# Optimization experiments

Hardware: AMD Instinct MI355X
Metric: run time of the kernel (lower is better)

Reference implementation:

```python
import jax, jax.numpy as jnp
import numpy as np

N_EXPERTS = 8
TOPK = 2
D_MODEL = 2048
D_FF = 2048
N_TOKENS = 8192
FP8_MAX = 448.0  # float8_e4m3fn max


def _fp8_quant_scalar(w):
    # per-tensor (scalar) fp8 quantization, as fp8_quantize(weight, scalar=True)
    amax = jnp.max(jnp.abs(w))
    scale = jnp.maximum(amax, 1e-12) / FP8_MAX
    q = (w / scale).astype(jnp.float8_e4m3fn).astype(jnp.float32)
    return q, scale


def _fp8_qdq_st(x):
    # dynamic_quant(x, single_scale=True) followed by inline dequant,
    # with straight-through estimator so fwd/bwd modules share math.
    amax = jnp.max(jnp.abs(x))
    scale = jnp.maximum(amax, 1e-12) / FP8_MAX
    qdq = (x / scale).astype(jnp.float8_e4m3fn).astype(jnp.float32) * scale
    return x + jax.lax.stop_gradient(qdq - x)


def setup_inputs() -> dict:
    key = jax.random.key(0)
    k1, k2, k3, k4 = jax.random.split(key, 4)
    x = jax.random.normal(k1, (N_TOKENS, D_MODEL), dtype=jnp.float32)
    gating_output = jax.random.normal(k2, (N_TOKENS, N_EXPERTS), dtype=jnp.float32)
    # per-expert fused gate+up weight [E, 2*d_ff, d_model], down weight [E, d_model, d_ff]
    w13 = jax.random.normal(k3, (N_EXPERTS, 2 * D_FF, D_MODEL), dtype=jnp.float32) * 0.02
    w2 = jax.random.normal(k4, (N_EXPERTS, D_MODEL, D_FF), dtype=jnp.float32) * 0.02
    w13_q, w13_scale = jax.vmap(_fp8_quant_scalar)(w13)
    w2_q, w2_scale = jax.vmap(_fp8_quant_scalar)(w2)
    return {
        "x": x,
        "gating_output": gating_output,
        "w13_q": w13_q,
        "w13_scale": w13_scale,
        "w2_q": w2_q,
        "w2_scale": w2_scale,
    }


def reference(x, gating_output, w13_q, w13_scale, w2_q, w2_scale):
    # --- select_experts: softmax scoring, top-k, renormalize ---
    probs = jax.nn.softmax(gating_output, axis=-1)              # [T, E]
    topk_w, topk_ids = jax.lax.top_k(probs, TOPK)               # [T, K]
    topk_w = topk_w / jnp.sum(topk_w, axis=-1, keepdims=True)   # renormalize=True

    # --- dynamic fp8 quantize + dequant of hidden states (single scale) ---
    x_dq = _fp8_qdq_st(x)                                       # [T, D]

    out = jnp.zeros((x.shape[0], D_MODEL), dtype=jnp.float32)
    for e in range(N_EXPERTS):
        # combine weight per token for this expert
        combine = jnp.sum(jnp.where(topk_ids == e, topk_w, 0.0), axis=-1)  # [T]
        w13 = w13_q[e] * w13_scale[e]                            # dequant [2F, D]
        w2 = w2_q[e] * w2_scale[e]                               # dequant [D, F]
        gu = x_dq @ w13.T                                        # [T, 2F]
        gate, up = gu[:, :D_FF], gu[:, D_FF:]
        h = jax.nn.silu(gate) * up                               # [T, F]
        out = out + combine[:, None] * (h @ w2.T)                # [T, D]
    return out
```

## Files before the change

### kernel.cpp

```cpp
#include <hip/hip_runtime.h>
#include <stdint.h>

#define T_TOK 8192
#define DM    2048
#define DFF   2048

typedef __attribute__((ext_vector_type(8))) short bf16x8;
typedef __attribute__((ext_vector_type(4))) float f32x4;

#define OFF_AMAX  0
#define OFF_CNT   64
#define OFF_PBASE 128
#define OFF_TMETA 192
#define OFF_TSE   256
#define OFF_TM0   960
#define OFF_BTOK  4096
#define OFF_BW    (OFF_BTOK + 16*T_TOK*4)
#define OFF_XQ    (2*1024*1024)
#define OFF_W13B  (OFF_XQ + T_TOK*DM*2)
#define OFF_W2B   (OFF_W13B + 8*2*DFF*DM*2)
#define OFF_H     (OFF_W2B + 8*DM*DFF*2)

#define GP(p) ((const __attribute__((address_space(1))) void*)(uintptr_t)(p))
#define LP(p) ((__attribute__((address_space(3))) void*)(uint32_t)(uintptr_t)(p))

__device__ __forceinline__ short bf16_rne(float f) {
    uint32_t b = __float_as_uint(f);
    b += 0x7FFFu + ((b >> 16) & 1u);
    return (short)(b >> 16);
}

__device__ __forceinline__ float fp8_round(float y) {
    float a = fabsf(y);
    a = fminf(a, 448.f);
    uint32_t b = __float_as_uint(a);
    if (b >= 0x3C800000u) {
        uint32_t lsb = (b >> 20) & 1u;
        b += 0x7FFFFu + lsb;
        b &= 0xFFF00000u;
        a = __uint_as_float(b);
    } else {
        a = rintf(a * 512.f) * (1.f / 512.f);
    }
    return (y < 0.f) ? -a : a;
}

__global__ void k_amax(const float4* __restrict__ x, unsigned* __restrict__ amax) {
    __shared__ float red[256];
    float m = 0.f;
    const int n4 = T_TOK * DM / 4;
    for (int i = blockIdx.x * blockDim.x + threadIdx.x; i < n4; i += gridDim.x * blockDim.x) {
        float4 v = x[i];
        m = fmaxf(m, fmaxf(fmaxf(fabsf(v.x), fabsf(v.y)), fmaxf(fabsf(v.z), fabsf(v.w))));
    }
    red[threadIdx.x] = m;
    __syncthreads();
    for (int s = 128; s > 0; s >>= 1) {
        if (threadIdx.x < s) red[threadIdx.x] = fmaxf(red[threadIdx.x], red[threadIdx.x + s]);
        __syncthreads();
    }
    if (threadIdx.x == 0) atomicMax(amax, __float_as_uint(red[0]));
}

__global__ void k_router(const float* __restrict__ gating, int* __restrict__ cnt,
                         int* __restrict__ btok, float* __restrict__ bw) {
    int t = blockIdx.x * blockDim.x + threadIdx.x;
    if (t >= T_TOK) return;
    float l[8], p[8];
    float lmax = -1e30f;
#pragma unroll
    for (int i = 0; i < 8; i++) { l[i] = gating[t * 8 + i]; lmax = fmaxf(lmax, l[i]); }
    float s = 0.f;
#pragma unroll
    for (int i = 0; i < 8; i++) { p[i] = __expf(l[i] - lmax); s += p[i]; }
    int i0 = 0;
#pragma unroll
    for (int i = 1; i < 8; i++) if (l[i] > l[i0]) i0 = i;
    int i1 = (i0 == 0) ? 1 : 0;
#pragma unroll
    for (int i = 0; i < 8; i++) if (i != i1 && i != i0 && l[i] > l[i1]) i1 = i;
    float pa = p[i0] / s, pb = p[i1] / s;
    float w0 = pa / (pa + pb), w1 = pb / (pa + pb);
    int pos = atomicAdd(&cnt[i0], 1);
    btok[i0 * T_TOK + pos] = t; bw[i0 * T_TOK + pos] = w0;
    pos = atomicAdd(&cnt[8 + i1], 1);
    btok[(8 + i1) * T_TOK + pos] = t; bw[(8 + i1) * T_TOK + pos] = w1;
}

__global__ void k_build(const int* __restrict__ cnt, int* __restrict__ pbase,
                        int* __restrict__ tmeta, int* __restrict__ tse, int* __restrict__ tm0) {
    if (threadIdx.x != 0 || blockIdx.x != 0) return;
    int base = 0, tt = 0, t0 = 0;
    for (int b = 0; b < 16; b++) {
        pbase[b] = base;
        int nt = (cnt[b] + 127) >> 7;
        for (int i = 0; i < nt; i++) { tse[tt] = b; tm0[tt] = i << 7; tt++; }
        base += nt << 7;
        if (b == 7) t0 = tt;
    }
    tmeta[0] = t0; tmeta[1] = tt;
}

__global__ void k_quant(const float4* __restrict__ x, short* __restrict__ xq,
                        const unsigned* __restrict__ amax) {
    float scale = fmaxf(__uint_as_float(*amax), 1e-12f) / 448.f;
    const int n4 = T_TOK * DM / 4;
    for (int i = blockIdx.x * blockDim.x + threadIdx.x; i < n4; i += gridDim.x * blockDim.x) {
        float4 v = x[i];
        short4 o;
        o.x = bf16_rne(fp8_round(v.x / scale));
        o.y = bf16_rne(fp8_round(v.y / scale));
        o.z = bf16_rne(fp8_round(v.z / scale));
        o.w = bf16_rne(fp8_round(v.w / scale));
        ((short4*)xq)[i] = o;
    }
}

__global__ void k_conv(const float4* __restrict__ w, short* __restrict__ o, int n4) {
    for (int i = blockIdx.x * blockDim.x + threadIdx.x; i < n4; i += gridDim.x * blockDim.x) {
        float4 v = w[i];
        short4 q;
        q.x = bf16_rne(v.x); q.y = bf16_rne(v.y); q.z = bf16_rne(v.z); q.w = bf16_rne(v.w);
        ((short4*)o)[i] = q;
    }
}

__launch_bounds__(256, 2)
__global__ void k_gemm1(const short* __restrict__ xq, const short* __restrict__ w13b,
                        short* __restrict__ hbuf, const char* __restrict__ ws,
                        const float* __restrict__ w13_scale) {
    const int* cnt   = (const int*)(ws + OFF_CNT);
    const int* pbase = (const int*)(ws + OFF_PBASE);
    const int* tmeta = (const int*)(ws + OFF_TMETA);
    const int* tse   = (const int*)(ws + OFF_TSE);
    const int* tm0a  = (const int*)(ws + OFF_TM0);
    const int* btok  = (const int*)(ws + OFF_BTOK);
    const float* bwt = (const float*)(ws + OFF_BW);

    int ti = blockIdx.y;
    if (ti >= tmeta[1]) return;
    const int b = tse[ti], m0 = tm0a[ti], e = b & 7, c_n = cnt[b];
    const int hbase = pbase[b] + m0;
    const int n0 = blockIdx.x * 64;

    const int tid = threadIdx.x, w = tid >> 6, l = tid & 63;
    __shared__ short sm[16384];

    const int rb = w * 8 + (l >> 3);
    const int gchunk = (l & 7) ^ (l >> 3);
    const int* btk = btok + b * T_TOK;
    const short* ap[4];
    const short* bp[4];
#pragma unroll
    for (int c = 0; c < 4; c++) {
        int r = c * 32 + rb;
        int rr = m0 + r; if (rr >= c_n) rr = c_n - 1;
        ap[c] = xq + (size_t)btk[rr] * DM + gchunk * 8;
        int wr = (r < 64) ? (n0 + r) : (DFF + n0 + (r - 64));
        bp[c] = w13b + (size_t)e * (2 * DFF) * DM + (size_t)wr * DM + gchunk * 8;
    }

    f32x4 zero = {0.f, 0.f, 0.f, 0.f};
    f32x4 acc[4][4];
#pragma unroll
    for (int i = 0; i < 4; i++)
#pragma unroll
        for (int j = 0; j < 4; j++) acc[i][j] = zero;

    const int mw = w & 1, nw = w >> 1;
    const int fr = l & 15, fk = l >> 4;

    for (int kt = 0; kt < 32; kt++) {
        const int ko = kt * 64;
#pragma unroll
        for (int c = 0; c < 4; c++)
            __builtin_amdgcn_global_load_lds(GP(ap[c] + ko), LP(sm + c * 2048 + w * 512), 16, 0, 0);
#pragma unroll
        for (int c = 0; c < 4; c++)
            __builtin_amdgcn_global_load_lds(GP(bp[c] + ko), LP(sm + 8192 + c * 2048 + w * 512), 16, 0, 0);
        asm volatile("s_waitcnt vmcnt(0)" ::: "memory");
        __syncthreads();
#pragma unroll
        for (int kk = 0; kk < 2; kk++) {
            const int g = kk * 4 + fk;
            bf16x8 af[4], bfr[4];
#pragma unroll
            for (int i = 0; i < 4; i++) {
                int row = mw * 64 + i * 16 + fr;
                af[i] = *(const bf16x8*)&sm[row * 64 + ((g ^ (row & 7)) << 3)];
            }
#pragma unroll
            for (int j = 0; j < 4; j++) {
                int row = nw * 64 + j * 16 + fr;
                bfr[j] = *(const bf16x8*)&sm[8192 + row * 64 + ((g ^ (row & 7)) << 3)];
            }
#pragma unroll
            for (int i = 0; i < 4; i++)
#pragma unroll
                for (int j = 0; j < 4; j++)
                    acc[i][j] = __builtin_amdgcn_mfma_f32_16x16x32_bf16(af[i], bfr[j], acc[i][j], 0, 0, 0);
        }
        __syncthreads();
    }

    const float sx = fmaxf(__uint_as_float(*(const unsigned*)(ws + OFF_AMAX)), 1e-12f) / 448.f;
    const float s1 = sx * w13_scale[e];
    float* U = (float*)sm;
    if (nw == 1) {
#pragma unroll
        for (int i = 0; i < 4; i++)
#pragma unroll
            for (int j = 0; j < 4; j++)
#pragma unroll
                for (int r = 0; r < 4; r++) {
                    int lm = i * 16 + fk * 4 + r, col = j * 16 + fr;
                    U[mw * 4096 + lm * 64 + col] = acc[i][j][r];
                }
    }
    __syncthreads();
    if (nw == 0) {
#pragma unroll
        for (int i = 0; i < 4; i++)
#pragma unroll
            for (int j = 0; j < 4; j++)
#pragma unroll
                for (int r = 0; r < 4; r++) {
                    int lml = i * 16 + fk * 4 + r;
                    int lm = mw * 64 + lml, col = j * 16 + fr;
                    float g = acc[i][j][r] * s1;
                    float u = U[mw * 4096 + lml * 64 + col] * s1;
                    float cc = (m0 + lm < c_n) ? bwt[b * T_TOK + m0 + lm] : 0.f;
                    float h = g / (1.f + __expf(-g)) * u * cc;
                    hbuf[(size_t)(hbase + lm) * DFF + n0 + col] = bf16_rne(h);
                }
    }
}

__launch_bounds__(256, 2)
__global__ void k_gemm2(const short* __restrict__ hbuf, const short* __restrict__ w2b,
                        float* __restrict__ out, const char* __restrict__ ws,
                        const float* __restrict__ w2_scale, const int slot) {
    const int* cnt   = (const int*)(ws + OFF_CNT);
    const int* pbase = (const int*)(ws + OFF_PBASE);
    const int* tmeta = (const int*)(ws + OFF_TMETA);
    const int* tse   = (const int*)(ws + OFF_TSE);
    const int* tm0a  = (const int*)(ws + OFF_TM0);
    const int* btok  = (const int*)(ws + OFF_BTOK);

    const int lo = slot ? tmeta[0] : 0;
    const int hi = slot ? tmeta[1] : tmeta[0];
    int ti = lo + blockIdx.y;
    if (ti >= hi) return;
    const int b = tse[ti], m0 = tm0a[ti], e = b & 7, c_n = cnt[b];
    const int hb = pbase[b] + m0;
    const int n0 = blockIdx.x * 128;

    const int tid = threadIdx.x, w = tid >> 6, l = tid & 63;
    __shared__ short sm[16384];

    const int rb = w * 8 + (l >> 3);
    const int gchunk = (l & 7) ^ (l >> 3);
    const short* ap[4];
    const short* bp[4];
#pragma unroll
    for (int c = 0; c < 4; c++) {
        int r = c * 32 + rb;
        ap[c] = hbuf + (size_t)(hb + r) * DFF + gchunk * 8;
        bp[c] = w2b + (size_t)e * DM * DFF + (size_t)(n0 + r) * DFF + gchunk * 8;
    }

    f32x4 zero = {0.f, 0.f, 0.f, 0.f};
    f32x4 acc[4][4];
#pragma unroll
    for (int i = 0; i < 4; i++)
#pragma unroll
        for (int j = 0; j < 4; j++) acc[i][j] = zero;

    const int mw = w & 1, nw = w >> 1;
    const int fr = l & 15, fk = l >> 4;

    for (int kt = 0; kt < 32; kt++) {
        const int ko = kt * 64;
#pragma unroll
        for (int c = 0; c < 4; c++)
            __builtin_amdgcn_global_load_lds(GP(ap[c] + ko), LP(sm + c * 2048 + w * 512), 16, 0, 0);
#pragma unroll
        for (int c = 0; c < 4; c++)
            __builtin_amdgcn_global_load_lds(GP(bp[c] + ko), LP(sm + 8192 + c * 2048 + w * 512), 16, 0, 0);
        asm volatile("s_waitcnt vmcnt(0)" ::: "memory");
        __syncthreads();
#pragma unroll
        for (int kk = 0; kk < 2; kk++) {
            const int g = kk * 4 + fk;
            bf16x8 af[4], bfr[4];
#pragma unroll
            for (int i = 0; i < 4; i++) {
                int row = mw * 64 + i * 16 + fr;
                af[i] = *(const bf16x8*)&sm[row * 64 + ((g ^ (row & 7)) << 3)];
            }
#pragma unroll
            for (int j = 0; j < 4; j++) {
                int row = nw * 64 + j * 16 + fr;
                bfr[j] = *(const bf16x8*)&sm[8192 + row * 64 + ((g ^ (row & 7)) << 3)];
            }
#pragma unroll
            for (int i = 0; i < 4; i++)
#pragma unroll
                for (int j = 0; j < 4; j++)
                    acc[i][j] = __builtin_amdgcn_mfma_f32_16x16x32_bf16(af[i], bfr[j], acc[i][j], 0, 0, 0);
        }
        __syncthreads();
    }

    const float s2 = w2_scale[e];
#pragma unroll
    for (int i = 0; i < 4; i++)
#pragma unroll
        for (int r = 0; r < 4; r++) {
            int lm = mw * 64 + i * 16 + fk * 4 + r;
            if (m0 + lm < c_n) {
                int tok = btok[b * T_TOK + m0 + lm];
#pragma unroll
                for (int j = 0; j < 4; j++) {
                    int col = n0 + nw * 64 + j * 16 + fr;
                    float v = acc[i][j][r] * s2;
                    float* o = out + (size_t)tok * DM + col;
                    if (slot) *o += v; else *o = v;
                }
            }
        }
}

extern "C" void kernel_launch(void* const* d_in, const int* in_sizes, int n_in,
                              void* d_out, int out_size, void* d_ws, size_t ws_size,
                              hipStream_t stream) {
    const float* x      = (const float*)d_in[0];
    const float* gating = (const float*)d_in[1];
    const float* w13q   = (const float*)d_in[2];
    const float* w13s   = (const float*)d_in[3];
    const float* w2q    = (const float*)d_in[4];
    const float* w2s    = (const float*)d_in[5];
    float* out = (float*)d_out;
    char* ws = (char*)d_ws;

    hipMemsetAsync(ws, 0, 4096, stream);
    k_amax<<<1024, 256, 0, stream>>>((const float4*)x, (unsigned*)(ws + OFF_AMAX));
    k_router<<<T_TOK / 256, 256, 0, stream>>>(gating, (int*)(ws + OFF_CNT),
                                              (int*)(ws + OFF_BTOK), (float*)(ws + OFF_BW));
    k_build<<<1, 64, 0, stream>>>((const int*)(ws + OFF_CNT), (int*)(ws + OFF_PBASE),
                                  (int*)(ws + OFF_TMETA), (int*)(ws + OFF_TSE), (int*)(ws + OFF_TM0));
    k_quant<<<1024, 256, 0, stream>>>((const float4*)x, (short*)(ws + OFF_XQ),
                                      (const unsigned*)(ws + OFF_AMAX));
    k_conv<<<2048, 256, 0, stream>>>((const float4*)w13q, (short*)(ws + OFF_W13B), 8 * 2 * DFF * DM / 4);
    k_conv<<<1024, 256, 0, stream>>>((const float4*)w2q, (short*)(ws + OFF_W2B), 8 * DM * DFF / 4);
    k_gemm1<<<dim3(32, 144), 256, 0, stream>>>((const short*)(ws + OFF_XQ), (const short*)(ws + OFF_W13B),
                                               (short*)(ws + OFF_H), ws, w13s);
    k_gemm2<<<dim3(16, 72), 256, 0, stream>>>((const short*)(ws + OFF_H), (const short*)(ws + OFF_W2B),
                                              out, ws, w2s, 0);
    k_gemm2<<<dim3(16, 72), 256, 0, stream>>>((const short*)(ws + OFF_H), (const short*)(ws + OFF_W2B),
                                              out, ws, w2s, 1);
}
```

Measured before the change: 1.148 ms.

## Run first expert GEMM in native FP8 MFMA and batch router atomics

Activations and w13 weights are now encoded as real e4m3 bytes instead of bf16-expanded values, and gemm1 uses the MX-scaled 16x16x128 f8f6f4 MFMA with unit scales. This halves the bytes loaded per tile and the quantize/convert write traffic, and doubles K per iteration. The router now aggregates per-block counts in shared memory before issuing one global atomic per bucket. The custom fp8 encoder depends on values already being fp8-representable, and any mismatch there would change the results.

```diff
diff --git a/kernel.cpp b/kernel.cpp
--- a/kernel.cpp
+++ b/kernel.cpp
@@ -7,6 +7,8 @@
 
 typedef __attribute__((ext_vector_type(8))) short bf16x8;
 typedef __attribute__((ext_vector_type(4))) float f32x4;
+typedef __attribute__((ext_vector_type(4))) int   i32x4;
+typedef __attribute__((ext_vector_type(8))) int   i32x8;
 
 #define OFF_AMAX  0
 #define OFF_CNT   64
@@ -17,8 +19,8 @@
 #define OFF_BTOK  4096
 #define OFF_BW    (OFF_BTOK + 16*T_TOK*4)
 #define OFF_XQ    (2*1024*1024)
-#define OFF_W13B  (OFF_XQ + T_TOK*DM*2)
-#define OFF_W2B   (OFF_W13B + 8*2*DFF*DM*2)
+#define OFF_W13F  (OFF_XQ + T_TOK*DM)
+#define OFF_W2B   (OFF_W13F + 8*2*DFF*DM)
 #define OFF_H     (OFF_W2B + 8*DM*DFF*2)
 
 #define GP(p) ((const __attribute__((address_space(1))) void*)(uintptr_t)(p))
@@ -45,6 +47,21 @@
     return (y < 0.f) ? -a : a;
 }
 
+__device__ __forceinline__ unsigned char fp8_enc(float v) {
+    uint32_t b = __float_as_uint(v);
+    uint32_t s = (b >> 24) & 0x80u;
+    float a = fabsf(v);
+    uint32_t q;
+    if (a < 0.015625f) {
+        q = (uint32_t)(a * 512.0f + 0.5f);
+    } else {
+        uint32_t e = (b >> 23) & 0xFFu;
+        uint32_t m = (b >> 20) & 7u;
+        q = ((e - 120u) << 3) | m;
+    }
+    return (unsigned char)(s | q);
+}
+
 __global__ void k_amax(const float4* __restrict__ x, unsigned* __restrict__ amax) {
     __shared__ float red[256];
     float m = 0.f;
@@ -64,8 +81,12 @@
 
 __global__ void k_router(const float* __restrict__ gating, int* __restrict__ cnt,
                          int* __restrict__ btok, float* __restrict__ bw) {
-    int t = blockIdx.x * blockDim.x + threadIdx.x;
-    if (t >= T_TOK) return;
+    __shared__ int lcnt[16];
+    __shared__ int lbase[16];
+    const int tid = threadIdx.x;
+    if (tid < 16) lcnt[tid] = 0;
+    __syncthreads();
+    const int t = blockIdx.x * 256 + tid;
     float l[8], p[8];
     float lmax = -1e30f;
 #pragma unroll
@@ -81,9 +102,14 @@
     for (int i = 0; i < 8; i++) if (i != i1 && i != i0 && l[i] > l[i1]) i1 = i;
     float pa = p[i0] / s, pb = p[i1] / s;
     float w0 = pa / (pa + pb), w1 = pb / (pa + pb);
-    int pos = atomicAdd(&cnt[i0], 1);
+    int p0 = atomicAdd(&lcnt[i0], 1);
+    int p1 = atomicAdd(&lcnt[8 + i1], 1);
+    __syncthreads();
+    if (tid < 16) lbase[tid] = atomicAdd(&cnt[tid], lcnt[tid]);
+    __syncthreads();
+    int pos = lbase[i0] + p0;
     btok[i0 * T_TOK + pos] = t; bw[i0 * T_TOK + pos] = w0;
-    pos = atomicAdd(&cnt[8 + i1], 1);
+    pos = lbase[8 + i1] + p1;
     btok[(8 + i1) * T_TOK + pos] = t; bw[(8 + i1) * T_TOK + pos] = w1;
 }
 
@@ -101,18 +127,27 @@
     tmeta[0] = t0; tmeta[1] = tt;
 }
 
-__global__ void k_quant(const float4* __restrict__ x, short* __restrict__ xq,
+__global__ void k_quant(const float4* __restrict__ x, unsigned char* __restrict__ xq,
                         const unsigned* __restrict__ amax) {
     float scale = fmaxf(__uint_as_float(*amax), 1e-12f) / 448.f;
     const int n4 = T_TOK * DM / 4;
     for (int i = blockIdx.x * blockDim.x + threadIdx.x; i < n4; i += gridDim.x * blockDim.x) {
         float4 v = x[i];
-        short4 o;
-        o.x = bf16_rne(fp8_round(v.x / scale));
-        o.y = bf16_rne(fp8_round(v.y / scale));
-        o.z = bf16_rne(fp8_round(v.z / scale));
-        o.w = bf16_rne(fp8_round(v.w / scale));
-        ((short4*)xq)[i] = o;
+        uchar4 o;
+        o.x = fp8_enc(fp8_round(v.x / scale));
+        o.y = fp8_enc(fp8_round(v.y / scale));
+        o.z = fp8_enc(fp8_round(v.z / scale));
+        o.w = fp8_enc(fp8_round(v.w / scale));
+        ((uchar4*)xq)[i] = o;
+    }
+}
+
+__global__ void k_conv13(const float4* __restrict__ w, unsigned char* __restrict__ o, int n4) {
+    for (int i = blockIdx.x * blockDim.x + threadIdx.x; i < n4; i += gridDim.x * blockDim.x) {
+        float4 v = w[i];
+        uchar4 q;
+        q.x = fp8_enc(v.x); q.y = fp8_enc(v.y); q.z = fp8_enc(v.z); q.w = fp8_enc(v.w);
+        ((uchar4*)o)[i] = q;
     }
 }
 
@@ -126,7 +161,7 @@
 }
 
 __launch_bounds__(256, 2)
-__global__ void k_gemm1(const short* __restrict__ xq, const short* __restrict__ w13b,
+__global__ void k_gemm1(const unsigned char* __restrict__ xq, const unsigned char* __restrict__ w13f,
                         short* __restrict__ hbuf, const char* __restrict__ ws,
                         const float* __restrict__ w13_scale) {
     const int* cnt   = (const int*)(ws + OFF_CNT);
@@ -144,20 +179,21 @@
     const int n0 = blockIdx.x * 64;
 
     const int tid = threadIdx.x, w = tid >> 6, l = tid & 63;
-    __shared__ short sm[16384];
+    __shared__ i32x4 smv[2048];
+    char* sm = (char*)smv;
 
     const int rb = w * 8 + (l >> 3);
     const int gchunk = (l & 7) ^ (l >> 3);
     const int* btk = btok + b * T_TOK;
-    const short* ap[4];
-    const short* bp[4];
+    const unsigned char* ap[4];
+    const unsigned char* bp[4];
 #pragma unroll
     for (int c = 0; c < 4; c++) {
         int r = c * 32 + rb;
         int rr = m0 + r; if (rr >= c_n) rr = c_n - 1;
-        ap[c] = xq + (size_t)btk[rr] * DM + gchunk * 8;
+        ap[c] = xq + (size_t)btk[rr] * DM + gchunk * 16;
         int wr = (r < 64) ? (n0 + r) : (DFF + n0 + (r - 64));
-        bp[c] = w13b + (size_t)e * (2 * DFF) * DM + (size_t)wr * DM + gchunk * 8;
+        bp[c] = w13f + (size_t)e * (2 * DFF) * DM + (size_t)wr * DM + gchunk * 16;
     }
 
     f32x4 zero = {0.f, 0.f, 0.f, 0.f};
@@ -170,36 +206,42 @@
     const int mw = w & 1, nw = w >> 1;
     const int fr = l & 15, fk = l >> 4;
 
-    for (int kt = 0; kt < 32; kt++) {
-        const int ko = kt * 64;
+    for (int kt = 0; kt < 16; kt++) {
+        const int ko = kt * 128;
 #pragma unroll
         for (int c = 0; c < 4; c++)
-            __builtin_amdgcn_global_load_lds(GP(ap[c] + ko), LP(sm + c * 2048 + w * 512), 16, 0, 0);
+            __builtin_amdgcn_global_load_lds(GP(ap[c] + ko), LP(sm + c * 4096 + w * 1024), 16, 0, 0);
 #pragma unroll
         for (int c = 0; c < 4; c++)
-            __builtin_amdgcn_global_load_lds(GP(bp[c] + ko), LP(sm + 8192 + c * 2048 + w * 512), 16, 0, 0);
+            __builtin_amdgcn_global_load_lds(GP(bp[c] + ko), LP(sm + 16384 + c * 4096 + w * 1024), 16, 0, 0);
         asm volatile("s_waitcnt vmcnt(0)" ::: "memory");
         __syncthreads();
-#pragma unroll
-        for (int kk = 0; kk < 2; kk++) {
-            const int g = kk * 4 + fk;
-            bf16x8 af[4], bfr[4];
-#pragma unroll
-            for (int i = 0; i < 4; i++) {
-                int row = mw * 64 + i * 16 + fr;
-                af[i] = *(const bf16x8*)&sm[row * 64 + ((g ^ (row & 7)) << 3)];
-            }
-#pragma unroll
-            for (int j = 0; j < 4; j++) {
-                int row = nw * 64 + j * 16 + fr;
-                bfr[j] = *(const bf16x8*)&sm[8192 + row * 64 + ((g ^ (row & 7)) << 3)];
-            }
-#pragma unroll
-            for (int i = 0; i < 4; i++)
-#pragma unroll
-                for (int j = 0; j < 4; j++)
-                    acc[i][j] = __builtin_amdgcn_mfma_f32_16x16x32_bf16(af[i], bfr[j], acc[i][j], 0, 0, 0);
+
+        i32x8 af[4], bf[4];
+#pragma unroll
+        for (int i = 0; i < 4; i++) {
+            int row = mw * 64 + i * 16 + fr;
+            const char* base = sm + row * 128;
+            i32x4 lo = *(const i32x4*)(base + ((((fk * 2)) ^ (row & 7)) << 4));
+            i32x4 hi = *(const i32x4*)(base + ((((fk * 2) | 1) ^ (row & 7)) << 4));
+            af[i][0] = lo[0]; af[i][1] = lo[1]; af[i][2] = lo[2]; af[i][3] = lo[3];
+            af[i][4] = hi[0]; af[i][5] = hi[1]; af[i][6] = hi[2]; af[i][7] = hi[3];
         }
+#pragma unroll
+        for (int j = 0; j < 4; j++) {
+            int row = nw * 64 + j * 16 + fr;
+            const char* base = sm + 16384 + row * 128;
+            i32x4 lo = *(const i32x4*)(base + ((((fk * 2)) ^ (row & 7)) << 4));
+            i32x4 hi = *(const i32x4*)(base + ((((fk * 2) | 1) ^ (row & 7)) << 4));
+            bf[j][0] = lo[0]; bf[j][1] = lo[1]; bf[j][2] = lo[2]; bf[j][3] = lo[3];
+            bf[j][4] = hi[0]; bf[j][5] = hi[1]; bf[j][6] = hi[2]; bf[j][7] = hi[3];
+        }
+#pragma unroll
+        for (int i = 0; i < 4; i++)
+#pragma unroll
+            for (int j = 0; j < 4; j++)
+                acc[i][j] = __builtin_amdgcn_mfma_scale_f32_16x16x128_f8f6f4(
+                    af[i], bf[j], acc[i][j], 0, 0, 0, 0x7F7F7F7F, 0, 0x7F7F7F7F);
         __syncthreads();
     }
 
@@ -256,7 +298,8 @@
     const int n0 = blockIdx.x * 128;
 
     const int tid = threadIdx.x, w = tid >> 6, l = tid & 63;
-    __shared__ short sm[16384];
+    __shared__ i32x4 smv2[2048];
+    short* sm = (short*)smv2;
 
     const int rb = w * 8 + (l >> 3);
     const int gchunk = (l & 7) ^ (l >> 3);
@@ -349,11 +392,13 @@
                                               (int*)(ws + OFF_BTOK), (float*)(ws + OFF_BW));
     k_build<<<1, 64, 0, stream>>>((const int*)(ws + OFF_CNT), (int*)(ws + OFF_PBASE),
                                   (int*)(ws + OFF_TMETA), (int*)(ws + OFF_TSE), (int*)(ws + OFF_TM0));
-    k_quant<<<1024, 256, 0, stream>>>((const float4*)x, (short*)(ws + OFF_XQ),
+    k_quant<<<1024, 256, 0, stream>>>((const float4*)x, (unsigned char*)(ws + OFF_XQ),
                                       (const unsigned*)(ws + OFF_AMAX));
-    k_conv<<<2048, 256, 0, stream>>>((const float4*)w13q, (short*)(ws + OFF_W13B), 8 * 2 * DFF * DM / 4);
+    k_conv13<<<2048, 256, 0, stream>>>((const float4*)w13q, (unsigned char*)(ws + OFF_W13F),
+                                       8 * 2 * DFF * DM / 4);
     k_conv<<<1024, 256, 0, stream>>>((const float4*)w2q, (short*)(ws + OFF_W2B), 8 * DM * DFF / 4);
-    k_gemm1<<<dim3(32, 144), 256, 0, stream>>>((const short*)(ws + OFF_XQ), (const short*)(ws + OFF_W13B),
+    k_gemm1<<<dim3(32, 144), 256, 0, stream>>>((const unsigned char*)(ws + OFF_XQ),
+                                               (const unsigned char*)(ws + OFF_W13F),
                                                (short*)(ws + OFF_H), ws, w13s);
     k_gemm2<<<dim3(16, 72), 256, 0, stream>>>((const short*)(ws + OFF_H), (const short*)(ws + OFF_W2B),
                                               out, ws, w2s, 0);
```

Result: faster. 987.7 us (-14.0%).
